# Performance work log

Measured on AMD Instinct MI355X. Metric: run time of the kernel, lower is better.

Reference implementation:

```python
import jax, jax.numpy as jnp
import numpy as np

# Renderer constants matching neural_renderer.Renderer(camera_mode='look',
# light_intensity_ambient=0.5, light_intensity_directional=0.5,
# light_direction=[0,0,1], viewing_angle=45) with image_size=256.
IMG = 256
TEX = 6
VIEW_ANGLE_DEG = 45.0
EYE = np.array([0.0, 0.0, -2.0], dtype=np.float32)          # camera position (look mode)
CAM_DIR = np.array([0.0, 0.0, 1.0], dtype=np.float32)       # camera_direction
CAM_UP = np.array([0.0, 1.0, 0.0], dtype=np.float32)        # camera_up
LIGHT_DIR = np.array([0.0, 0.0, 1.0], dtype=np.float32)
AMBIENT = 0.5
DIRECTIONAL = 0.5
EPS = 1e-8


def setup_inputs() -> dict:
    key = jax.random.key(0)
    k1, k2, k3 = jax.random.split(key, 3)
    # mesh roughly centered at origin; camera sits at z=-2 looking toward +z
    vertices = 0.5 * jax.random.normal(k1, (1, 400, 3), dtype=jnp.float32)
    faces = jax.random.randint(k2, (1, 640, 3), 0, 400, dtype=jnp.int64)
    textures = 0.5 * jax.random.normal(k3, (1, 640, TEX, TEX, TEX, 3), dtype=jnp.float32)
    return {"vertices": vertices, "faces": faces, "textures": textures}


def _normalize(v):
    return v / (jnp.linalg.norm(v, axis=-1, keepdims=True) + EPS)


def reference(vertices, faces, textures):
    v = vertices[0]                 # [N,3]
    f = faces[0]                    # [F,3] int
    tex = jnp.tanh(textures[0])     # [F,T,T,T,3]  (torch.tanh(textures))

    fv = v[f]                       # [F,3,3] per-face vertex positions (world)

    # ---- lighting (ambient + directional, white lights) ----
    n = jnp.cross(fv[:, 1] - fv[:, 0], fv[:, 2] - fv[:, 0])  # [F,3]
    n = _normalize(n)
    diff = jax.nn.relu(n @ jnp.asarray(LIGHT_DIR))           # [F]
    light = AMBIENT + DIRECTIONAL * diff                     # [F] (same for rgb)

    # ---- 'look' camera transform ----
    z_ax = _normalize(jnp.asarray(CAM_DIR))
    x_ax = _normalize(jnp.cross(jnp.asarray(CAM_UP), z_ax))
    y_ax = jnp.cross(z_ax, x_ax)
    R = jnp.stack([x_ax, y_ax, z_ax], axis=0)                # [3,3]
    vc = (fv - jnp.asarray(EYE)) @ R.T                       # [F,3,3] camera space

    # ---- perspective projection ----
    wfov = jnp.tan(jnp.deg2rad(VIEW_ANGLE_DEG)).astype(jnp.float32)
    zc = vc[..., 2]                                          # [F,3] depth
    xy = vc[..., :2] / (zc[..., None] * wfov + EPS)          # [F,3,2] in [-1,1]

    # ---- rasterize: barycentric coords per pixel per face ----
    ps = (jnp.arange(IMG, dtype=jnp.float32) + 0.5) / IMG * 2.0 - 1.0
    px, py = jnp.meshgrid(ps, -ps, indexing="xy")            # image y flipped
    pts = jnp.stack([px.ravel(), py.ravel()], axis=-1)       # [P,2]

    v0 = xy[:, 0]                                            # [F,2]
    d = xy[:, 1] - v0                                        # [F,2]
    e = xy[:, 2] - v0                                        # [F,2]
    det = d[:, 0] * e[:, 1] - d[:, 1] * e[:, 0]              # [F]
    det_ok = jnp.abs(det) > 1e-8
    det_s = jnp.where(det_ok, det, 1.0)

    q = pts[:, None, :] - v0[None, :, :]                     # [P,F,2]
    w1 = (q[..., 0] * e[:, 1] - q[..., 1] * e[:, 0]) / det_s # [P,F]
    w2 = (d[:, 0] * q[..., 1] - d[:, 1] * q[..., 0]) / det_s # [P,F]
    w0 = 1.0 - w1 - w2

    inside = (w0 >= 0) & (w1 >= 0) & (w2 >= 0) & det_ok[None, :]
    depth = w0 * zc[:, 0] + w1 * zc[:, 1] + w2 * zc[:, 2]    # [P,F]
    visible = inside & (depth > 0)

    # ---- z-buffer: nearest visible face per pixel ----
    big = jnp.float32(1e30)
    dmask = jnp.where(visible, depth, big)                   # [P,F]
    idx = jnp.argmin(dmask, axis=1)                          # [P]
    valid = jnp.take_along_axis(visible, idx[:, None], axis=1)[:, 0]  # [P]

    gather = lambda a: jnp.take_along_axis(a, idx[:, None], axis=1)[:, 0]
    b0, b1, b2 = gather(w0), gather(w1), gather(w2)          # [P] each

    # ---- texture lookup: nearest cell in TxTxT cube by barycentric coords ----
    ti = lambda b: jnp.clip((b * TEX).astype(jnp.int32), 0, TEX - 1)
    i0, i1, i2 = ti(b0), ti(b1), ti(b2)
    col = tex[idx, i0, i1, i2]                               # [P,3]
    col = col * light[idx][:, None]                          # shade

    img = jnp.where(valid[:, None], col, 0.0)                # [P,3]
    img = img.reshape(IMG, IMG, 3).transpose(2, 0, 1)[None]  # [1,3,H,W]
    return img
```

## Files before the change

### kernel.cpp

```cpp
#include <hip/hip_runtime.h>
#include <math.h>

#define NF   640
#define IMGN 256
#define NPIX (IMGN * IMGN)
#define TEXN 6
#define TPB  512
#define PXW  64
#define NCH  8
#define CHF  (NF / NCH)

__global__ __launch_bounds__(TPB) void render_kernel(
    const float* __restrict__ verts,
    const int*   __restrict__ faces,
    const float* __restrict__ tex,
    float* __restrict__ out)
{
#pragma clang fp contract(off)
    __shared__ float4 fAB[NF * 2];
    __shared__ float4 fC[NF];
    __shared__ unsigned short sList[NCH][CHF];
    __shared__ float rD[NCH][PXW];
    __shared__ int   rI[NCH][PXW];

    const float EPSf = 1e-8f;
    const int tid  = (int)threadIdx.x;
    const int wid  = tid >> 6;
    const int lane = tid & 63;
    const int p0   = (int)blockIdx.x * PXW;
    const int pi   = p0 >> 8;
    const int pj0  = p0 & (IMGN - 1);

    const float by    = -(((pi + 0.5f) / (float)IMGN) * 2.0f - 1.0f);
    const float bxmin = ((pj0 + 0.5f) / (float)IMGN) * 2.0f - 1.0f;
    const float bxmax = ((pj0 + (PXW - 1) + 0.5f) / (float)IMGN) * 2.0f - 1.0f;

    const int fbeg = wid * CHF;
    int cnt = 0;
    for (int r = 0; r < 2; ++r) {
        int idx = r * 64 + lane;
        int f = fbeg + idx;
        bool pred = false;
        if (idx < CHF) {
            int ia = faces[3 * f + 0];
            int ib = faces[3 * f + 1];
            int ic = faces[3 * f + 2];
            float ax = verts[3 * ia], ay = verts[3 * ia + 1], az = verts[3 * ia + 2];
            float bx = verts[3 * ib], byy = verts[3 * ib + 1], bz = verts[3 * ib + 2];
            float cx = verts[3 * ic], cy = verts[3 * ic + 1], cz = verts[3 * ic + 2];

            float e1x = bx - ax, e1y = byy - ay, e1z = bz - az;
            float e2x = cx - ax, e2y = cy - ay, e2z = cz - az;
            float nx = e1y * e2z - e1z * e2y;
            float ny = e1z * e2x - e1x * e2z;
            float nz = e1x * e2y - e1y * e2x;
            float nn = sqrtf((nx * nx + ny * ny) + nz * nz) + EPSf;
            float diff = nz / nn;
            diff = diff > 0.0f ? diff : 0.0f;
            float light = 0.5f + 0.5f * diff;

            float z0 = az + 2.0f, z1 = bz + 2.0f, z2 = cz + 2.0f;
            float den0 = z0 * 1.0f + EPSf;
            float den1 = z1 * 1.0f + EPSf;
            float den2 = z2 * 1.0f + EPSf;
            float px0 = ax / den0, py0 = ay / den0;
            float px1 = bx / den1, py1 = byy / den1;
            float px2 = cx / den2, py2 = cy / den2;

            float dx = px1 - px0, dy = py1 - py0;
            float ex = px2 - px0, ey = py2 - py0;
            float det = dx * ey - dy * ex;
            bool ok = fabsf(det) > 1e-8f;

            fAB[2 * f]     = make_float4(px0, py0, ex, ey);
            fAB[2 * f + 1] = make_float4(dx, dy, ok ? det : 1.0f, z0);
            fC[f]          = make_float4(z1, z2, light, 0.0f);

            if (ok) {
                float xmin = fminf(px0, fminf(px1, px2));
                float xmax = fmaxf(px0, fmaxf(px1, px2));
                float ymin = fminf(py0, fminf(py1, py2));
                float ymax = fmaxf(py0, fmaxf(py1, py2));
                float padx = (fmaxf(fabsf(xmin), fabsf(xmax)) + 1.0f) * 1e-6f;
                float pady = (fmaxf(fabsf(ymin), fabsf(ymax)) + 1.0f) * 1e-6f;
                pred = (xmin - padx <= bxmax) && (xmax + padx >= bxmin) &&
                       (ymin - pady <= by)    && (ymax + pady >= by);
            }
        }
        unsigned long long m = __ballot(pred);
        if (pred)
            sList[wid][cnt + (int)__popcll(m & ((1ull << lane) - 1ull))] =
                (unsigned short)f;
        cnt += (int)__popcll(m);
    }

    const float ppx = ((pj0 + lane + 0.5f) / (float)IMGN) * 2.0f - 1.0f;
    const float ppy = by;

    float best = 1e30f;
    int   bi = -1;

    for (int k = 0; k < cnt; ++k) {
        int f = (int)sList[wid][k];
        float4 a = fAB[2 * f];
        float4 b = fAB[2 * f + 1];
        float qx = ppx - a.x;
        float qy = ppy - a.y;
        float n1 = qx * a.w - qy * a.z;
        float n2 = b.x * qy - b.y * qx;
        bool pass = (b.z > 0.0f) ? (n1 >= 0.0f && n2 >= 0.0f)
                                 : (n1 <= 0.0f && n2 <= 0.0f);
        if (pass) {
            float w1 = n1 / b.z;
            float w2 = n2 / b.z;
            float w0 = (1.0f - w1) - w2;
            if (w0 >= 0.0f) {
                float4 c = fC[f];
                float depth = ((w0 * b.w) + (w1 * c.x)) + (w2 * c.y);
                if (depth > 0.0f && depth < best) {
                    best = depth; bi = f;
                }
            }
        }
    }

    rD[wid][lane] = best;
    rI[wid][lane] = bi;
    __syncthreads();

    if (tid < PXW) {
        float bd = rD[0][tid];
        int   fi = rI[0][tid];
        for (int c = 1; c < NCH; ++c) {
            float d = rD[c][tid];
            if (d < bd) { bd = d; fi = rI[c][tid]; }
        }

        int pp = p0 + tid;
        float r = 0.0f, g = 0.0f, b = 0.0f;
        if (fi >= 0) {
            float4 a2 = fAB[2 * fi];
            float4 b2 = fAB[2 * fi + 1];
            float sx = ((pj0 + tid + 0.5f) / (float)IMGN) * 2.0f - 1.0f;
            float qx = sx - a2.x;
            float qy = by - a2.y;
            float n1 = qx * a2.w - qy * a2.z;
            float n2 = b2.x * qy - b2.y * qx;
            float w1 = n1 / b2.z;
            float w2 = n2 / b2.z;
            float w0 = (1.0f - w1) - w2;

            int i0 = (int)(w0 * (float)TEXN);
            int i1 = (int)(w1 * (float)TEXN);
            int i2 = (int)(w2 * (float)TEXN);
            i0 = i0 < 0 ? 0 : (i0 > TEXN - 1 ? TEXN - 1 : i0);
            i1 = i1 < 0 ? 0 : (i1 > TEXN - 1 ? TEXN - 1 : i1);
            i2 = i2 < 0 ? 0 : (i2 > TEXN - 1 ? TEXN - 1 : i2);
            const float* tp = tex + (size_t)((((fi * TEXN + i0) * TEXN + i1) * TEXN + i2) * 3);
            float light = fC[fi].z;
            r = tanhf(tp[0]) * light;
            g = tanhf(tp[1]) * light;
            b = tanhf(tp[2]) * light;
        }
        out[pp]            = r;
        out[NPIX + pp]     = g;
        out[2 * NPIX + pp] = b;
    }
}

extern "C" void kernel_launch(void* const* d_in, const int* in_sizes, int n_in,
                              void* d_out, int out_size, void* d_ws, size_t ws_size,
                              hipStream_t stream) {
    (void)in_sizes; (void)n_in; (void)d_ws; (void)ws_size; (void)out_size;
    const float* verts = (const float*)d_in[0];
    const int*   faces = (const int*)d_in[1];
    const float* tex   = (const float*)d_in[2];
    float*       out   = (float*)d_out;
    render_kernel<<<NPIX / PXW, TPB, 0, stream>>>(verts, faces, tex, out);
}
```

Measured before the change: 27.45 us.

## Precompute per-face setup in a separate kernel and share via workspace

Moves the per-face projection, lighting and bounding-box computation out of the render kernel into a small setup kernel that writes records to the workspace. Each of the 1024 render blocks then copies those precomputed records into shared memory and culls against stored bounding boxes, instead of recomputing all 640 faces with gathers and divides. This removes redundant per-block arithmetic and scattered vertex loads, at the cost of an extra kernel launch with a dependency between the two kernels.

Result: slower. 30.94 us (+12.7%).

```diff
diff --git a/kernel.cpp b/kernel.cpp
--- a/kernel.cpp
+++ b/kernel.cpp
@@ -10,20 +10,76 @@
 #define NCH  8
 #define CHF  (NF / NCH)
 
-__global__ __launch_bounds__(TPB) void render_kernel(
+
+__global__ __launch_bounds__(256) void setup_kernel(
     const float* __restrict__ verts,
     const int*   __restrict__ faces,
+    float4* __restrict__ ws)
+{
+#pragma clang fp contract(off)
+    int f = (int)(blockIdx.x * 256 + threadIdx.x);
+    if (f >= NF) return;
+    const float EPSf = 1e-8f;
+
+    int ia = faces[3 * f + 0];
+    int ib = faces[3 * f + 1];
+    int ic = faces[3 * f + 2];
+    float ax = verts[3 * ia], ay = verts[3 * ia + 1], az = verts[3 * ia + 2];
+    float bx = verts[3 * ib], by = verts[3 * ib + 1], bz = verts[3 * ib + 2];
+    float cx = verts[3 * ic], cy = verts[3 * ic + 1], cz = verts[3 * ic + 2];
+
+    float e1x = bx - ax, e1y = by - ay, e1z = bz - az;
+    float e2x = cx - ax, e2y = cy - ay, e2z = cz - az;
+    float nx = e1y * e2z - e1z * e2y;
+    float ny = e1z * e2x - e1x * e2z;
+    float nz = e1x * e2y - e1y * e2x;
+    float nn = sqrtf((nx * nx + ny * ny) + nz * nz) + EPSf;
+    float diff = nz / nn;
+    diff = diff > 0.0f ? diff : 0.0f;
+    float light = 0.5f + 0.5f * diff;
+
+    float z0 = az + 2.0f, z1 = bz + 2.0f, z2 = cz + 2.0f;
+    float den0 = z0 * 1.0f + EPSf;
+    float den1 = z1 * 1.0f + EPSf;
+    float den2 = z2 * 1.0f + EPSf;
+    float px0 = ax / den0, py0 = ay / den0;
+    float px1 = bx / den1, py1 = by / den1;
+    float px2 = cx / den2, py2 = cy / den2;
+
+    float dx = px1 - px0, dy = py1 - py0;
+    float ex = px2 - px0, ey = py2 - py0;
+    float det = dx * ey - dy * ex;
+    bool ok = fabsf(det) > 1e-8f;
+
+    ws[2 * f + 0]  = make_float4(px0, py0, ex, ey);
+    ws[2 * f + 1]  = make_float4(dx, dy, ok ? det : 1.0f, z0);
+    ws[1280 + f]   = make_float4(z1, z2, light, 0.0f);
+
+    if (ok) {
+        float xmin = fminf(px0, fminf(px1, px2));
+        float xmax = fmaxf(px0, fmaxf(px1, px2));
+        float ymin = fminf(py0, fminf(py1, py2));
+        float ymax = fmaxf(py0, fmaxf(py1, py2));
+        float padx = (fmaxf(fabsf(xmin), fabsf(xmax)) + 1.0f) * 1e-6f;
+        float pady = (fmaxf(fabsf(ymin), fabsf(ymax)) + 1.0f) * 1e-6f;
+        ws[1920 + f] = make_float4(xmin - padx, xmax + padx,
+                                   ymin - pady, ymax + pady);
+    } else {
+        ws[1920 + f] = make_float4(3e30f, -3e30f, 3e30f, -3e30f);
+    }
+}
+
+__global__ __launch_bounds__(TPB) void render_kernel(
+    const float4* __restrict__ ws,
     const float* __restrict__ tex,
     float* __restrict__ out)
 {
 #pragma clang fp contract(off)
-    __shared__ float4 fAB[NF * 2];
-    __shared__ float4 fC[NF];
+    __shared__ float4 rec[1920];
     __shared__ unsigned short sList[NCH][CHF];
     __shared__ float rD[NCH][PXW];
     __shared__ int   rI[NCH][PXW];
 
-    const float EPSf = 1e-8f;
     const int tid  = (int)threadIdx.x;
     const int wid  = tid >> 6;
     const int lane = tid & 63;
@@ -34,6 +90,12 @@
     const float by    = -(((pi + 0.5f) / (float)IMGN) * 2.0f - 1.0f);
     const float bxmin = ((pj0 + 0.5f) / (float)IMGN) * 2.0f - 1.0f;
     const float bxmax = ((pj0 + (PXW - 1) + 0.5f) / (float)IMGN) * 2.0f - 1.0f;
+
+    #pragma unroll
+    for (int r = 0; r < 4; ++r) {
+        int i = r * TPB + tid;
+        if (i < 1920) rec[i] = ws[i];
+    }
 
     const int fbeg = wid * CHF;
     int cnt = 0;
@@ -42,50 +104,9 @@
         int f = fbeg + idx;
         bool pred = false;
         if (idx < CHF) {
-            int ia = faces[3 * f + 0];
-            int ib = faces[3 * f + 1];
-            int ic = faces[3 * f + 2];
-            float ax = verts[3 * ia], ay = verts[3 * ia + 1], az = verts[3 * ia + 2];
-            float bx = verts[3 * ib], byy = verts[3 * ib + 1], bz = verts[3 * ib + 2];
-            float cx = verts[3 * ic], cy = verts[3 * ic + 1], cz = verts[3 * ic + 2];
-
-            float e1x = bx - ax, e1y = byy - ay, e1z = bz - az;
-            float e2x = cx - ax, e2y = cy - ay, e2z = cz - az;
-            float nx = e1y * e2z - e1z * e2y;
-            float ny = e1z * e2x - e1x * e2z;
-            float nz = e1x * e2y - e1y * e2x;
-            float nn = sqrtf((nx * nx + ny * ny) + nz * nz) + EPSf;
-            float diff = nz / nn;
-            diff = diff > 0.0f ? diff : 0.0f;
-            float light = 0.5f + 0.5f * diff;
-
-            float z0 = az + 2.0f, z1 = bz + 2.0f, z2 = cz + 2.0f;
-            float den0 = z0 * 1.0f + EPSf;
-            float den1 = z1 * 1.0f + EPSf;
-            float den2 = z2 * 1.0f + EPSf;
-            float px0 = ax / den0, py0 = ay / den0;
-            float px1 = bx / den1, py1 = byy / den1;
-            float px2 = cx / den2, py2 = cy / den2;
-
-            float dx = px1 - px0, dy = py1 - py0;
-            float ex = px2 - px0, ey = py2 - py0;
-            float det = dx * ey - dy * ex;
-            bool ok = fabsf(det) > 1e-8f;
-
-            fAB[2 * f]     = make_float4(px0, py0, ex, ey);
-            fAB[2 * f + 1] = make_float4(dx, dy, ok ? det : 1.0f, z0);
-            fC[f]          = make_float4(z1, z2, light, 0.0f);
-
-            if (ok) {
-                float xmin = fminf(px0, fminf(px1, px2));
-                float xmax = fmaxf(px0, fmaxf(px1, px2));
-                float ymin = fminf(py0, fminf(py1, py2));
-                float ymax = fmaxf(py0, fmaxf(py1, py2));
-                float padx = (fmaxf(fabsf(xmin), fabsf(xmax)) + 1.0f) * 1e-6f;
-                float pady = (fmaxf(fabsf(ymin), fabsf(ymax)) + 1.0f) * 1e-6f;
-                pred = (xmin - padx <= bxmax) && (xmax + padx >= bxmin) &&
-                       (ymin - pady <= by)    && (ymax + pady >= by);
-            }
+            float4 bb = ws[1920 + f];
+            pred = (bb.x <= bxmax) && (bb.y >= bxmin) &&
+                   (bb.z <= by)    && (bb.w >= by);
         }
         unsigned long long m = __ballot(pred);
         if (pred)
@@ -93,6 +114,7 @@
                 (unsigned short)f;
         cnt += (int)__popcll(m);
     }
+    __syncthreads();
 
     const float ppx = ((pj0 + lane + 0.5f) / (float)IMGN) * 2.0f - 1.0f;
     const float ppy = by;
@@ -102,8 +124,8 @@
 
     for (int k = 0; k < cnt; ++k) {
         int f = (int)sList[wid][k];
-        float4 a = fAB[2 * f];
-        float4 b = fAB[2 * f + 1];
+        float4 a = rec[2 * f];
+        float4 b = rec[2 * f + 1];
         float qx = ppx - a.x;
         float qy = ppy - a.y;
         float n1 = qx * a.w - qy * a.z;
@@ -115,7 +137,7 @@
             float w2 = n2 / b.z;
             float w0 = (1.0f - w1) - w2;
             if (w0 >= 0.0f) {
-                float4 c = fC[f];
+                float4 c = rec[1280 + f];
                 float depth = ((w0 * b.w) + (w1 * c.x)) + (w2 * c.y);
                 if (depth > 0.0f && depth < best) {
                     best = depth; bi = f;
@@ -139,8 +161,8 @@
         int pp = p0 + tid;
         float r = 0.0f, g = 0.0f, b = 0.0f;
         if (fi >= 0) {
-            float4 a2 = fAB[2 * fi];
-            float4 b2 = fAB[2 * fi + 1];
+            float4 a2 = rec[2 * fi];
+            float4 b2 = rec[2 * fi + 1];
             float sx = ((pj0 + tid + 0.5f) / (float)IMGN) * 2.0f - 1.0f;
             float qx = sx - a2.x;
             float qy = by - a2.y;
@@ -157,7 +179,7 @@
             i1 = i1 < 0 ? 0 : (i1 > TEXN - 1 ? TEXN - 1 : i1);
             i2 = i2 < 0 ? 0 : (i2 > TEXN - 1 ? TEXN - 1 : i2);
             const float* tp = tex + (size_t)((((fi * TEXN + i0) * TEXN + i1) * TEXN + i2) * 3);
-            float light = fC[fi].z;
+            float light = rec[1280 + fi].z;
             r = tanhf(tp[0]) * light;
             g = tanhf(tp[1]) * light;
             b = tanhf(tp[2]) * light;
@@ -171,10 +193,13 @@
 extern "C" void kernel_launch(void* const* d_in, const int* in_sizes, int n_in,
                               void* d_out, int out_size, void* d_ws, size_t ws_size,
                               hipStream_t stream) {
-    (void)in_sizes; (void)n_in; (void)d_ws; (void)ws_size; (void)out_size;
+    (void)in_sizes; (void)n_in; (void)ws_size; (void)out_size;
     const float* verts = (const float*)d_in[0];
     const int*   faces = (const int*)d_in[1];
     const float* tex   = (const float*)d_in[2];
     float*       out   = (float*)d_out;
-    render_kernel<<<NPIX / PXW, TPB, 0, stream>>>(verts, faces, tex, out);
+    float4*      ws    = (float4*)d_ws;
+
+    setup_kernel<<<(NF + 255) / 256, 256, 0, stream>>>(verts, faces, ws);
+    render_kernel<<<NPIX / PXW, TPB, 0, stream>>>(ws, tex, out);
 }
```

## Process a full image row per block with four pixels per lane

Applied to the files above, without the earlier changes.

Each block now renders an entire 256-pixel row instead of a 64-pixel segment, with each lane evaluating four pixels per candidate face. This amortizes the per-block face projection, lighting and culling setup over more pixels and reuses the loaded face data and y-dependent terms across four pixels. In exchange the culling only tests the row's y-range, so candidate lists grow, and the grid shrinks to 256 blocks, which may reduce occupancy across the device.

After: 47.10 us. 1.72x slower.

```diff
diff --git a/kernel.cpp b/kernel.cpp
--- a/kernel.cpp
+++ b/kernel.cpp
@@ -6,9 +6,9 @@
 #define NPIX (IMGN * IMGN)
 #define TEXN 6
 #define TPB  512
-#define PXW  64
 #define NCH  8
 #define CHF  (NF / NCH)
+#define PPL  4
 
 __global__ __launch_bounds__(TPB) void render_kernel(
     const float* __restrict__ verts,
@@ -20,20 +20,18 @@
     __shared__ float4 fAB[NF * 2];
     __shared__ float4 fC[NF];
     __shared__ unsigned short sList[NCH][CHF];
-    __shared__ float rD[NCH][PXW];
-    __shared__ int   rI[NCH][PXW];
+    __shared__ float rD[NCH][IMGN];
+    __shared__ int   rI[NCH][IMGN];
 
     const float EPSf = 1e-8f;
     const int tid  = (int)threadIdx.x;
     const int wid  = tid >> 6;
     const int lane = tid & 63;
-    const int p0   = (int)blockIdx.x * PXW;
-    const int pi   = p0 >> 8;
-    const int pj0  = p0 & (IMGN - 1);
+    const int row  = (int)blockIdx.x;
 
-    const float by    = -(((pi + 0.5f) / (float)IMGN) * 2.0f - 1.0f);
-    const float bxmin = ((pj0 + 0.5f) / (float)IMGN) * 2.0f - 1.0f;
-    const float bxmax = ((pj0 + (PXW - 1) + 0.5f) / (float)IMGN) * 2.0f - 1.0f;
+    const float by    = -(((row + 0.5f) / (float)IMGN) * 2.0f - 1.0f);
+    const float bxmin = ((0   + 0.5f) / (float)IMGN) * 2.0f - 1.0f;
+    const float bxmax = ((255 + 0.5f) / (float)IMGN) * 2.0f - 1.0f;
 
     const int fbeg = wid * CHF;
     int cnt = 0;
@@ -83,8 +81,8 @@
                 float ymax = fmaxf(py0, fmaxf(py1, py2));
                 float padx = (fmaxf(fabsf(xmin), fabsf(xmax)) + 1.0f) * 1e-6f;
                 float pady = (fmaxf(fabsf(ymin), fabsf(ymax)) + 1.0f) * 1e-6f;
-                pred = (xmin - padx <= bxmax) && (xmax + padx >= bxmin) &&
-                       (ymin - pady <= by)    && (ymax + pady >= by);
+                pred = (ymin - pady <= by)    && (ymax + pady >= by) &&
+                       (xmin - padx <= bxmax) && (xmax + padx >= bxmin);
             }
         }
         unsigned long long m = __ballot(pred);
@@ -93,55 +91,68 @@
                 (unsigned short)f;
         cnt += (int)__popcll(m);
     }
+    __syncthreads();
 
-    const float ppx = ((pj0 + lane + 0.5f) / (float)IMGN) * 2.0f - 1.0f;
-    const float ppy = by;
+    float ppx[PPL];
+    float best[PPL];
+    int   bi[PPL];
+    #pragma unroll
+    for (int k = 0; k < PPL; ++k) {
+        ppx[k]  = ((lane + 64 * k + 0.5f) / (float)IMGN) * 2.0f - 1.0f;
+        best[k] = 1e30f;
+        bi[k]   = -1;
+    }
 
-    float best = 1e30f;
-    int   bi = -1;
-
-    for (int k = 0; k < cnt; ++k) {
-        int f = (int)sList[wid][k];
+    for (int kk = 0; kk < cnt; ++kk) {
+        int f = (int)sList[wid][kk];
         float4 a = fAB[2 * f];
         float4 b = fAB[2 * f + 1];
-        float qx = ppx - a.x;
-        float qy = ppy - a.y;
-        float n1 = qx * a.w - qy * a.z;
-        float n2 = b.x * qy - b.y * qx;
-        bool pass = (b.z > 0.0f) ? (n1 >= 0.0f && n2 >= 0.0f)
-                                 : (n1 <= 0.0f && n2 <= 0.0f);
-        if (pass) {
-            float w1 = n1 / b.z;
-            float w2 = n2 / b.z;
-            float w0 = (1.0f - w1) - w2;
-            if (w0 >= 0.0f) {
-                float4 c = fC[f];
-                float depth = ((w0 * b.w) + (w1 * c.x)) + (w2 * c.y);
-                if (depth > 0.0f && depth < best) {
-                    best = depth; bi = f;
+        float4 c = fC[f];
+        float qy  = by - a.y;
+        float t1  = qy * a.z;
+        float t2  = b.x * qy;
+        #pragma unroll
+        for (int k = 0; k < PPL; ++k) {
+            float qx = ppx[k] - a.x;
+            float n1 = qx * a.w - t1;
+            float n2 = t2 - b.y * qx;
+            bool pass = (b.z > 0.0f) ? (n1 >= 0.0f && n2 >= 0.0f)
+                                     : (n1 <= 0.0f && n2 <= 0.0f);
+            if (pass) {
+                float w1 = n1 / b.z;
+                float w2 = n2 / b.z;
+                float w0 = (1.0f - w1) - w2;
+                if (w0 >= 0.0f) {
+                    float depth = ((w0 * b.w) + (w1 * c.x)) + (w2 * c.y);
+                    if (depth > 0.0f && depth < best[k]) {
+                        best[k] = depth; bi[k] = f;
+                    }
                 }
             }
         }
     }
 
-    rD[wid][lane] = best;
-    rI[wid][lane] = bi;
+    #pragma unroll
+    for (int k = 0; k < PPL; ++k) {
+        rD[wid][lane + 64 * k] = best[k];
+        rI[wid][lane + 64 * k] = bi[k];
+    }
     __syncthreads();
 
-    if (tid < PXW) {
+    if (tid < IMGN) {
         float bd = rD[0][tid];
         int   fi = rI[0][tid];
-        for (int c = 1; c < NCH; ++c) {
-            float d = rD[c][tid];
-            if (d < bd) { bd = d; fi = rI[c][tid]; }
+        for (int cc = 1; cc < NCH; ++cc) {
+            float d = rD[cc][tid];
+            if (d < bd) { bd = d; fi = rI[cc][tid]; }
         }
 
-        int pp = p0 + tid;
+        int pp = row * IMGN + tid;
         float r = 0.0f, g = 0.0f, b = 0.0f;
         if (fi >= 0) {
             float4 a2 = fAB[2 * fi];
             float4 b2 = fAB[2 * fi + 1];
-            float sx = ((pj0 + tid + 0.5f) / (float)IMGN) * 2.0f - 1.0f;
+            float sx = ((tid + 0.5f) / (float)IMGN) * 2.0f - 1.0f;
             float qx = sx - a2.x;
             float qy = by - a2.y;
             float n1 = qx * a2.w - qy * a2.z;
@@ -176,5 +187,5 @@
     const int*   faces = (const int*)d_in[1];
     const float* tex   = (const float*)d_in[2];
     float*       out   = (float*)d_out;
-    render_kernel<<<NPIX / PXW, TPB, 0, stream>>>(verts, faces, tex, out);
+    render_kernel<<<IMGN, TPB, 0, stream>>>(verts, faces, tex, out);
 }
```
